# Kernel tuning notes

Measured on AMD Instinct MI355X. Metric: run time of the kernel, lower is better.

The kernel has to match this reference:

```python
import jax, jax.numpy as jnp
import numpy as np
import math

D_INNER = 512
D_STATE = 16
DT_RANK = 32
B_SZ = 2
L_SEQ = 4096


def setup_inputs() -> dict:
    key = jax.random.key(0)
    ks = jax.random.split(key, 6)
    x = jax.random.normal(ks[0], (B_SZ, L_SEQ, D_INNER), dtype=jnp.float32)
    # parameters (match torch init semantics closely enough for a numeric baseline)
    A = jnp.arange(1, D_STATE + 1, dtype=jnp.float32)
    A_log = jnp.broadcast_to(jnp.log(A)[None, :], (D_INNER, D_STATE)).copy()
    D_param = jnp.ones((D_INNER,), dtype=jnp.float32)
    # x_proj: Linear(d_inner -> dt_rank + 2*d_state), no bias
    W_xproj = jax.random.normal(ks[1], (DT_RANK + 2 * D_STATE, D_INNER), dtype=jnp.float32) / np.sqrt(D_INNER)
    # dt_proj: Linear(dt_rank -> d_inner) with special bias init
    W_dt = jax.random.normal(ks[2], (D_INNER, DT_RANK), dtype=jnp.float32) / np.sqrt(DT_RANK)
    dt_init = jnp.exp(jax.random.uniform(ks[3], (D_INNER,)) * (math.log(0.1) - math.log(0.001)) + math.log(0.001))
    b_dt = jnp.log(jnp.exp(dt_init) - 1.0)
    alpha = jnp.asarray(0.6, dtype=jnp.float32)
    beta_logit = jnp.asarray(math.log(0.99 / (1.0 - 0.99 + 1e-08)), dtype=jnp.float32)
    return {"x": x, "A_log": A_log, "D_param": D_param, "W_xproj": W_xproj,
            "W_dt": W_dt, "b_dt": b_dt, "alpha": alpha, "beta_logit": beta_logit}


def _momentum_ssm(x, A_log, D_param, W_xproj, W_dt, b_dt, alpha, beta_logit):
    # x: (B, L, D)
    proj = jnp.einsum('bld,pd->blp', x, W_xproj)            # (B, L, r+2N)
    dt_in = proj[..., :DT_RANK]
    Bp = proj[..., DT_RANK:DT_RANK + D_STATE]                # (B, L, N)
    Cp = proj[..., DT_RANK + D_STATE:]                       # (B, L, N)
    dt = jax.nn.softplus(jnp.einsum('blr,dr->bld', dt_in, W_dt) + b_dt)  # (B, L, D)
    A = -jnp.exp(A_log)                                      # (D, N)
    A_bar = jnp.exp(dt[..., None] * A[None, None])           # (B, L, D, N)
    # fused B_bar * x_t: dt * Bp * x
    inp = dt[..., None] * Bp[:, :, None, :] * x[..., None]   # (B, L, D, N)
    beta = jax.nn.sigmoid(beta_logit)

    # scan over time; carry (h, v): (B, D, N)
    h0 = jnp.zeros((x.shape[0], D_INNER, D_STATE), dtype=x.dtype)
    v0 = jnp.zeros_like(h0)

    def step(carry, ts):
        h, v = carry
        a_t, inp_t, c_t = ts                                 # (B,D,N), (B,D,N), (B,N)
        v = beta * v + alpha * inp_t
        h = a_t * h + v
        y = jnp.einsum('bdn,bn->bd', h, c_t)
        return (h, v), y

    xs = (jnp.moveaxis(A_bar, 1, 0), jnp.moveaxis(inp, 1, 0), jnp.moveaxis(Cp, 1, 0))
    _, ys = jax.lax.scan(step, (h0, v0), xs)                 # ys: (L, B, D)
    y = jnp.moveaxis(ys, 0, 1)                               # (B, L, D)
    return y + D_param * x


def reference(x, A_log, D_param, W_xproj, W_dt, b_dt, alpha, beta_logit):
    return _momentum_ssm(x, A_log, D_param, W_xproj, W_dt, b_dt, alpha, beta_logit)
```

## Files before the change

### kernel.cpp

```cpp
#include <hip/hip_runtime.h>


#define D_IN 512
#define D_ST 16
#define DTR  32
#define BSZ  2
#define LSEQ 4096
#define PDIM 64
#define NCH  256
#define LCH  (LSEQ / NCH)
#define LOG2E 1.44269504f
#define LN2   0.69314718f

typedef __attribute__((ext_vector_type(8))) short short8;
typedef __attribute__((ext_vector_type(4))) float f32x4;
typedef _Float16 f16;
typedef __attribute__((ext_vector_type(8))) _Float16 f16x8;

__device__ inline float fast_exp2(float x) { return __builtin_amdgcn_exp2f(x); }
__device__ inline float fast_log2(float x) { return __builtin_amdgcn_logf(x); }

__device__ inline unsigned short bf16_rne(float f) {
  unsigned b = __float_as_uint(f);
  return (unsigned short)((b + 0x7fffu + ((b >> 16) & 1u)) >> 16);
}

__device__ inline void cvt8(const float4 u, const float4 v, short8& hi, short8& lo) {
  float f[8] = {u.x, u.y, u.z, u.w, v.x, v.y, v.z, v.w};
#pragma unroll
  for (int i = 0; i < 8; ++i) {
    unsigned short h = bf16_rne(f[i]);
    hi[i] = (short)h;
    float r = f[i] - __uint_as_float((unsigned)h << 16);
    lo[i] = (short)bf16_rne(r);
  }
}

__device__ inline void st16h(f16* p, const float* s) {
  f16 t[16];
#pragma unroll
  for (int i = 0; i < 16; ++i) t[i] = (f16)s[i];
  *(f16x8*)p = *(f16x8*)&t[0];
  *(f16x8*)(p + 8) = *(f16x8*)&t[8];
}
__device__ inline void ld16h(const f16* p, float* d) {
  f16x8 a = *(const f16x8*)p;
  f16x8 b = *(const f16x8*)(p + 8);
#pragma unroll
  for (int i = 0; i < 8; ++i) { d[i] = (float)a[i]; d[8 + i] = (float)b[i]; }
}

#define PWCHK(val, n)                                                        \
  pw = pw && (fabsf((val) - (float)((n) + 1) * a0) <=                        \
              2e-5f * fabsf((float)((n) + 1) * a0));

__device__ inline bool detectA2(const float* __restrict__ A_log, int d, float& a0) {
  const float4* ap = (const float4*)(A_log + (size_t)d * D_ST);
  float4 r0 = ap[0], r1 = ap[1], r2 = ap[2], r3 = ap[3];
  float4 e0 = make_float4(-__expf(r0.x) * LOG2E, -__expf(r0.y) * LOG2E,
                          -__expf(r0.z) * LOG2E, -__expf(r0.w) * LOG2E);
  float4 e1 = make_float4(-__expf(r1.x) * LOG2E, -__expf(r1.y) * LOG2E,
                          -__expf(r1.z) * LOG2E, -__expf(r1.w) * LOG2E);
  float4 e2 = make_float4(-__expf(r2.x) * LOG2E, -__expf(r2.y) * LOG2E,
                          -__expf(r2.z) * LOG2E, -__expf(r2.w) * LOG2E);
  float4 e3 = make_float4(-__expf(r3.x) * LOG2E, -__expf(r3.y) * LOG2E,
                          -__expf(r3.z) * LOG2E, -__expf(r3.w) * LOG2E);
  a0 = e0.x;
  bool pw = true;
  PWCHK(e0.y, 1) PWCHK(e0.z, 2) PWCHK(e0.w, 3)
  PWCHK(e1.x, 4) PWCHK(e1.y, 5) PWCHK(e1.z, 6) PWCHK(e1.w, 7)
  PWCHK(e2.x, 8) PWCHK(e2.y, 9) PWCHK(e2.z, 10) PWCHK(e2.w, 11)
  PWCHK(e3.x, 12) PWCHK(e3.y, 13) PWCHK(e3.z, 14) PWCHK(e3.w, 15)
  return pw;
}

__global__ __launch_bounds__(256) void k_wprep(const float* __restrict__ W,
                                               short* __restrict__ Whi,
                                               short* __restrict__ Wlo) {
  const int i = (blockIdx.x * 256 + threadIdx.x) * 4;
  float4 w = *(const float4*)(W + i);
  float f[4] = {w.x, w.y, w.z, w.w};
  unsigned short h[4], lo[4];
#pragma unroll
  for (int j = 0; j < 4; ++j) {
    h[j] = bf16_rne(f[j]);
    float r = f[j] - __uint_as_float((unsigned)h[j] << 16);
    lo[j] = bf16_rne(r);
  }
  *(uint2*)(Whi + i) = make_uint2(h[0] | ((unsigned)h[1] << 16), h[2] | ((unsigned)h[3] << 16));
  *(uint2*)(Wlo + i) = make_uint2(lo[0] | ((unsigned)lo[1] << 16), lo[2] | ((unsigned)lo[3] << 16));
}

#define MM3(ACC, AH, AL, BH, BL)                                        \
  ACC = __builtin_amdgcn_mfma_f32_16x16x32_bf16(AL, BH, ACC, 0, 0, 0);  \
  ACC = __builtin_amdgcn_mfma_f32_16x16x32_bf16(AH, BL, ACC, 0, 0, 0);  \
  ACC = __builtin_amdgcn_mfma_f32_16x16x32_bf16(AH, BH, ACC, 0, 0, 0);

#define LOADB(P, S)                                   \
  {                                                   \
    const int kb = (S) * 32;                          \
    P##h0 = *(const short8*)(bh + kb);                \
    P##h1 = *(const short8*)(bh + 8192 + kb);         \
    P##h2 = *(const short8*)(bh + 16384 + kb);        \
    P##h3 = *(const short8*)(bh + 24576 + kb);        \
    P##l0 = *(const short8*)(bl + kb);                \
    P##l1 = *(const short8*)(bl + 8192 + kb);         \
    P##l2 = *(const short8*)(bl + 16384 + kb);        \
    P##l3 = *(const short8*)(bl + 24576 + kb);        \
  }

#define LOADA(Aa, Ab, S)                              \
  {                                                   \
    const int ka = (S) * 32;                          \
    Aa = *(const float4*)(xr + ka);                   \
    Ab = *(const float4*)(xr + ka + 4);               \
  }

#define COMPSTEP(Aa, Ab, P)                           \
  {                                                   \
    short8 ahi, alo;                                  \
    cvt8(Aa, Ab, ahi, alo);                           \
    MM3(acc0, ahi, alo, P##h0, P##l0);                \
    MM3(acc1, ahi, alo, P##h1, P##l1);                \
    MM3(acc2, ahi, alo, P##h2, P##l2);                \
    MM3(acc3, ahi, alo, P##h3, P##l3);                \
  }

__global__ __launch_bounds__(256) void k_proj(const float* __restrict__ x,
                                              const short* __restrict__ Whi,
                                              const short* __restrict__ Wlo,
                                              float* __restrict__ proj) {
  __shared__ float Pacc[4][16][64];
  const int row0 = blockIdx.x * 16;
  const int l = threadIdx.x & 63;
  const int wq = threadIdx.x >> 6;
  const int m = l & 15;
  const int ko = (l >> 4) * 8 + wq * 128;
  const float* xr = x + (size_t)(row0 + m) * D_IN + ko;
  const short* bh = Whi + (size_t)m * D_IN + ko;
  const short* bl = Wlo + (size_t)m * D_IN + ko;

  f32x4 acc0 = {0.f, 0.f, 0.f, 0.f}, acc1 = acc0, acc2 = acc0, acc3 = acc0;
  float4 A0a, A0b, A1a, A1b, A2a, A2b, A3a, A3b;
  short8 Xh0, Xh1, Xh2, Xh3, Xl0, Xl1, Xl2, Xl3;
  short8 Yh0, Yh1, Yh2, Yh3, Yl0, Yl1, Yl2, Yl3;
  LOADA(A0a, A0b, 0); LOADA(A1a, A1b, 1); LOADA(A2a, A2b, 2); LOADA(A3a, A3b, 3);
  LOADB(X, 0); LOADB(Y, 1);

  COMPSTEP(A0a, A0b, X); LOADB(X, 2);
  COMPSTEP(A1a, A1b, Y); LOADB(Y, 3);
  COMPSTEP(A2a, A2b, X);
  COMPSTEP(A3a, A3b, Y);

  const int r0 = (l >> 4) * 4;
#pragma unroll
  for (int r = 0; r < 4; ++r) {
    Pacc[wq][r0 + r][m] = acc0[r];
    Pacc[wq][r0 + r][16 + m] = acc1[r];
    Pacc[wq][r0 + r][32 + m] = acc2[r];
    Pacc[wq][r0 + r][48 + m] = acc3[r];
  }
  __syncthreads();

  const int orow = threadIdx.x >> 4;
  const int ocol = (threadIdx.x & 15) * 4;
  float4 s0 = *(const float4*)&Pacc[0][orow][ocol];
  float4 s1 = *(const float4*)&Pacc[1][orow][ocol];
  float4 s2 = *(const float4*)&Pacc[2][orow][ocol];
  float4 s3 = *(const float4*)&Pacc[3][orow][ocol];
  float4 o = make_float4((s0.x + s1.x) + (s2.x + s3.x), (s0.y + s1.y) + (s2.y + s3.y),
                         (s0.z + s1.z) + (s2.z + s3.z), (s0.w + s1.w) + (s2.w + s3.w));
  *(float4*)(proj + (size_t)(row0 + orow) * PDIM + ocol) = o;
}

#define S1_LOOP                                                              \
  _Pragma("unroll")                                                          \
  for (int j = 0; j < LCH; ++j) {                                            \
    const float4* pj = (const float4*)(pb + j * PDIM);                       \
    float4 pp[8];                                                            \
    _Pragma("unroll")                                                        \
    for (int k = 0; k < 8; ++k) pp[k] = pj[k];                               \
    float c0 = bb, c1 = 0.f, c2 = 0.f, c3 = 0.f;                             \
    _Pragma("unroll")                                                        \
    for (int k = 0; k < 8; ++k) {                                            \
      c0 = fmaf(pp[k].x, w4[k].x, c0);                                       \
      c1 = fmaf(pp[k].y, w4[k].y, c1);                                       \
      c2 = fmaf(pp[k].z, w4[k].z, c2);                                       \
      c3 = fmaf(pp[k].w, w4[k].w, c3);                                       \
    }                                                                        \
    const float acc = (c0 + c1) + (c2 + c3);                                 \
    const float ee = fast_exp2(acc * LOG2E);                                 \
    const float dtc = (acc > 20.f) ? acc : LN2 * fast_log2(1.f + ee);        \
    dp[(size_t)j * D_IN] = (f16)dtc;                                         \
    sd += dtc;                                                               \
    bpow *= beta;                                                            \
    const float u = alpha * dtc * xs[j];                                     \
    float4 bq[4];                                                            \
    _Pragma("unroll")                                                        \
    for (int k = 0; k < 4; ++k) bq[k] = pj[8 + k];                           \
    const float* Bf = (const float*)bq;                                      \
    AR_INIT;                                                                 \
    _Pragma("unroll")                                                        \
    for (int n = 0; n < 16; ++n) {                                           \
      AR_STEP;                                                               \
      v[n] = fmaf(beta, v[n], u * Bf[n]);                                    \
      h[n] = fmaf(ar, h[n], v[n]);                                           \
      cv[n] = fmaf(ar, cv[n], bpow);                                         \
    }                                                                        \
  }

__global__ __launch_bounds__(256) void k_scan1(const float* __restrict__ x,
                                               const float* __restrict__ proj,
                                               const float* __restrict__ A_log,
                                               const float* __restrict__ W_dt,
                                               const float* __restrict__ b_dt,
                                               const float* __restrict__ alpha_p,
                                               const float* __restrict__ beta_p,
                                               f16* __restrict__ hh,
                                               f16* __restrict__ vh,
                                               f16* __restrict__ cvv,
                                               float* __restrict__ sdt,
                                               f16* __restrict__ dth) {
  const int c = blockIdx.x, b = blockIdx.z;
  const int d = blockIdx.y * 256 + threadIdx.x;
  const int t0 = c * LCH;
  const float* pb = proj + ((size_t)b * LSEQ + t0) * PDIM;

  float xs[LCH];
  {
    const float* xp = x + ((size_t)b * LSEQ + t0) * D_IN + d;
#pragma unroll
    for (int j = 0; j < LCH; ++j) xs[j] = xp[(size_t)j * D_IN];
  }
  float4 w4[8];
  {
    const float4* wp = (const float4*)(W_dt + (size_t)d * DTR);
#pragma unroll
    for (int i = 0; i < 8; ++i) w4[i] = wp[i];
  }
  const float bb = b_dt[d];
  const float alpha = alpha_p[0];
  const float beta = 1.f / (1.f + __expf(-beta_p[0]));
  float a0;
  const bool pw = detectA2(A_log, d, a0);

  f16* dp = dth + ((size_t)b * LSEQ + t0) * D_IN + d;
  float h[16] = {}, v[16] = {}, cv[16] = {};
  float bpow = 1.f, sd = 0.f;

  if (pw) {
#define AR_INIT const float r = fast_exp2(dtc * a0); float ar = 1.f
#define AR_STEP ar *= r
    S1_LOOP
#undef AR_INIT
#undef AR_STEP
  } else {
    volatile const float* av = A_log + (size_t)d * D_ST;
#define AR_INIT float ar
#define AR_STEP ar = fast_exp2(dtc * (-__expf(av[n]) * LOG2E))
    S1_LOOP
#undef AR_INIT
#undef AR_STEP
  }

  const size_t base = ((size_t)(b * NCH + c) * D_IN + d) * D_ST;
  st16h(hh + base, h);
  st16h(vh + base, v);
  st16h(cvv + base, cv);
  sdt[(size_t)(b * NCH + c) * D_IN + d] = sd;
}

__global__ __launch_bounds__(64) void k_fix(f16* __restrict__ hh,
                                            f16* __restrict__ vh,
                                            const f16* __restrict__ cvv,
                                            const float* __restrict__ sdt,
                                            const float* __restrict__ A_log,
                                            const float* __restrict__ beta_p) {
  const int g = blockIdx.x * 64 + threadIdx.x;
  const int b = g >> 13;
  const int dn = g & 8191;
  const float beta = 1.f / (1.f + __expf(-beta_p[0]));
  const float A2 = -__expf(A_log[dn]) * LOG2E;
  float bL = beta;
#pragma unroll
  for (int i = 0; i < 4; ++i) bL *= bL;

  const size_t cs = (size_t)D_IN * D_ST;
  const size_t base = (size_t)b * NCH * cs + dn;
  const size_t sbase = (size_t)b * NCH * D_IN + (dn >> 4);

  float hg[16], vg[16], cg[16], sg[16];
#pragma unroll
  for (int i = 0; i < 16; ++i) {
    hg[i] = (float)hh[base + i * cs];
    vg[i] = (float)vh[base + i * cs];
    cg[i] = (float)cvv[base + i * cs];
    sg[i] = sdt[sbase + i * D_IN];
  }
  float H = 0.f, V = 0.f;
  for (int c0 = 0; c0 < NCH; c0 += 16) {
    const int cp = (c0 + 16) & (NCH - 1);
    float hn[16], vn[16], cn[16], sn[16];
#pragma unroll
    for (int i = 0; i < 16; ++i) {
      hn[i] = (float)hh[base + (size_t)(cp + i) * cs];
      vn[i] = (float)vh[base + (size_t)(cp + i) * cs];
      cn[i] = (float)cvv[base + (size_t)(cp + i) * cs];
      sn[i] = sdt[sbase + (size_t)(cp + i) * D_IN];
    }
#pragma unroll
    for (int i = 0; i < 16; ++i) {
      hh[base + (size_t)(c0 + i) * cs] = (f16)H;
      vh[base + (size_t)(c0 + i) * cs] = (f16)V;
      const float Pa = fast_exp2(sg[i] * A2);
      const float Hn = fmaf(Pa, H, fmaf(cg[i], V, hg[i]));
      V = fmaf(bL, V, vg[i]);
      H = Hn;
    }
#pragma unroll
    for (int i = 0; i < 16; ++i) { hg[i] = hn[i]; vg[i] = vn[i]; cg[i] = cn[i]; sg[i] = sn[i]; }
  }
}

#define S2_LOOP                                                              \
  _Pragma("unroll")                                                          \
  for (int j = 0; j < LCH; ++j) {                                            \
    const float4* pj = (const float4*)(pb + j * PDIM);                       \
    float4 bq[8];                                                            \
    _Pragma("unroll")                                                        \
    for (int k = 0; k < 8; ++k) bq[k] = pj[8 + k];                           \
    const float* Bf = (const float*)bq;                                      \
    const float dtc = dtv[j], xv = xs[j];                                    \
    const float u = alpha * dtc * xv;                                        \
    float y0 = 0.f, y1 = 0.f, y2 = 0.f, y3 = 0.f;                            \
    AR_INIT;                                                                 \
    _Pragma("unroll")                                                        \
    for (int n = 0; n < 16; ++n) {                                           \
      AR_STEP;                                                               \
      v[n] = fmaf(beta, v[n], u * Bf[n]);                                    \
      h[n] = fmaf(ar, h[n], v[n]);                                           \
      float hc = h[n] * Bf[16 + n];                                          \
      if ((n & 3) == 0) y0 += hc;                                            \
      else if ((n & 3) == 1) y1 += hc;                                       \
      else if ((n & 3) == 2) y2 += hc;                                       \
      else y3 += hc;                                                         \
    }                                                                        \
    op[(size_t)j * D_IN] = (y0 + y1) + (y2 + y3) + Dv * xv;                  \
  }

__global__ __launch_bounds__(256) void k_scan2(const float* __restrict__ x,
                                               const f16* __restrict__ dth,
                                               const float* __restrict__ proj,
                                               const float* __restrict__ A_log,
                                               const float* __restrict__ D_param,
                                               const float* __restrict__ alpha_p,
                                               const float* __restrict__ beta_p,
                                               const f16* __restrict__ hh,
                                               const f16* __restrict__ vh,
                                               float* __restrict__ out) {
  const int c = blockIdx.x, b = blockIdx.z;
  const int d = blockIdx.y * 256 + threadIdx.x;
  const int t0 = c * LCH;
  const float* pb = proj + ((size_t)b * LSEQ + t0) * PDIM;

  float xs[LCH], dtv[LCH];
  {
    const float* xp = x + ((size_t)b * LSEQ + t0) * D_IN + d;
    const f16* dp = dth + ((size_t)b * LSEQ + t0) * D_IN + d;
#pragma unroll
    for (int j = 0; j < LCH; ++j) xs[j] = xp[(size_t)j * D_IN];
#pragma unroll
    for (int j = 0; j < LCH; ++j) dtv[j] = (float)dp[(size_t)j * D_IN];
  }
  const float alpha = alpha_p[0];
  const float beta = 1.f / (1.f + __expf(-beta_p[0]));
  const float Dv = D_param[d];
  float a0;
  const bool pw = detectA2(A_log, d, a0);
  const size_t ibase = ((size_t)(b * NCH + c) * D_IN + d) * D_ST;
  float h[16], v[16];
  ld16h(hh + ibase, h);
  ld16h(vh + ibase, v);

  float* op = out + ((size_t)b * LSEQ + t0) * D_IN + d;
  if (pw) {
#define AR_INIT const float r = fast_exp2(dtc * a0); float ar = 1.f
#define AR_STEP ar *= r
    S2_LOOP
#undef AR_INIT
#undef AR_STEP
  } else {
    volatile const float* av = A_log + (size_t)d * D_ST;
#define AR_INIT float ar
#define AR_STEP ar = fast_exp2(dtc * (-__expf(av[n]) * LOG2E))
    S2_LOOP
#undef AR_INIT
#undef AR_STEP
  }
}

extern "C" void kernel_launch(void* const* d_in, const int* in_sizes, int n_in,
                              void* d_out, int out_size, void* d_ws, size_t ws_size,
                              hipStream_t stream) {
  const float* x = (const float*)d_in[0];
  const float* A_log = (const float*)d_in[1];
  const float* D_param = (const float*)d_in[2];
  const float* W_xproj = (const float*)d_in[3];
  const float* W_dt = (const float*)d_in[4];
  const float* b_dt = (const float*)d_in[5];
  const float* alpha = (const float*)d_in[6];
  const float* beta_logit = (const float*)d_in[7];
  float* out = (float*)d_out;

  const size_t NST = (size_t)BSZ * NCH * D_IN * D_ST;
  float* ws = (float*)d_ws;
  float* proj = ws;
  float* sdt = proj + (size_t)BSZ * LSEQ * PDIM;
  f16* hh = (f16*)(sdt + (size_t)BSZ * NCH * D_IN);
  f16* vh = hh + NST;
  f16* cvv = vh + NST;
  f16* dth = cvv + NST;
  short* Whi = (short*)(dth + (size_t)BSZ * LSEQ * D_IN);
  short* Wlo = Whi + (size_t)PDIM * D_IN;

  k_wprep<<<dim3(PDIM * D_IN / 1024), dim3(256), 0, stream>>>(W_xproj, Whi, Wlo);
  k_proj<<<dim3(BSZ * LSEQ / 16), dim3(256), 0, stream>>>(x, Whi, Wlo, proj);
  k_scan1<<<dim3(NCH, D_IN / 256, BSZ), dim3(256), 0, stream>>>(
      x, proj, A_log, W_dt, b_dt, alpha, beta_logit, hh, vh, cvv, sdt, dth);
  k_fix<<<dim3(BSZ * D_IN * D_ST / 64), dim3(64), 0, stream>>>(hh, vh, cvv, sdt, A_log,
                                                               beta_logit);
  k_scan2<<<dim3(NCH, D_IN / 256, BSZ), dim3(256), 0, stream>>>(
      x, dth, proj, A_log, D_param, alpha, beta_logit, hh, vh, out);
}
```

Measured before the change: 167.8 us.

## Fuse x_proj GEMM into both chunked scan kernels via shared memory

Removes the standalone projection kernel and its global proj buffer. Each scan block now handles all 512 channels of one chunk with 512 threads, computes the 16x64 projection tile for its chunk using split-bf16 MFMA into shared memory, then reads B/C/dt_in from LDS. The projection is recomputed in both scan passes, trading extra MFMA work and a block-level sync against one kernel launch and a global round trip. Block count halves while block size doubles, which changes occupancy.

```diff
diff --git a/kernel.cpp b/kernel.cpp
--- a/kernel.cpp
+++ b/kernel.cpp
@@ -96,87 +96,48 @@
   ACC = __builtin_amdgcn_mfma_f32_16x16x32_bf16(AH, BL, ACC, 0, 0, 0);  \
   ACC = __builtin_amdgcn_mfma_f32_16x16x32_bf16(AH, BH, ACC, 0, 0, 0);
 
-#define LOADB(P, S)                                   \
-  {                                                   \
-    const int kb = (S) * 32;                          \
-    P##h0 = *(const short8*)(bh + kb);                \
-    P##h1 = *(const short8*)(bh + 8192 + kb);         \
-    P##h2 = *(const short8*)(bh + 16384 + kb);        \
-    P##h3 = *(const short8*)(bh + 24576 + kb);        \
-    P##l0 = *(const short8*)(bl + kb);                \
-    P##l1 = *(const short8*)(bl + 8192 + kb);         \
-    P##l2 = *(const short8*)(bl + 16384 + kb);        \
-    P##l3 = *(const short8*)(bl + 24576 + kb);        \
-  }
-
-#define LOADA(Aa, Ab, S)                              \
-  {                                                   \
-    const int ka = (S) * 32;                          \
-    Aa = *(const float4*)(xr + ka);                   \
-    Ab = *(const float4*)(xr + ka + 4);               \
-  }
-
-#define COMPSTEP(Aa, Ab, P)                           \
-  {                                                   \
-    short8 ahi, alo;                                  \
-    cvt8(Aa, Ab, ahi, alo);                           \
-    MM3(acc0, ahi, alo, P##h0, P##l0);                \
-    MM3(acc1, ahi, alo, P##h1, P##l1);                \
-    MM3(acc2, ahi, alo, P##h2, P##l2);                \
-    MM3(acc3, ahi, alo, P##h3, P##l3);                \
-  }
-
-__global__ __launch_bounds__(256) void k_proj(const float* __restrict__ x,
-                                              const short* __restrict__ Whi,
-                                              const short* __restrict__ Wlo,
-                                              float* __restrict__ proj) {
-  __shared__ float Pacc[4][16][64];
-  const int row0 = blockIdx.x * 16;
+__device__ inline void stage_proj(const float* __restrict__ x,
+                                  const short* __restrict__ Whi,
+                                  const short* __restrict__ Wlo,
+                                  int b, int t0,
+                                  float (*Pacc)[16][64], float (*Ps)[64]) {
   const int l = threadIdx.x & 63;
-  const int wq = threadIdx.x >> 6;
+  const int w = threadIdx.x >> 6;
+  const int q = w & 3, kh = w >> 2;
   const int m = l & 15;
-  const int ko = (l >> 4) * 8 + wq * 128;
-  const float* xr = x + (size_t)(row0 + m) * D_IN + ko;
-  const short* bh = Whi + (size_t)m * D_IN + ko;
-  const short* bl = Wlo + (size_t)m * D_IN + ko;
-
-  f32x4 acc0 = {0.f, 0.f, 0.f, 0.f}, acc1 = acc0, acc2 = acc0, acc3 = acc0;
-  float4 A0a, A0b, A1a, A1b, A2a, A2b, A3a, A3b;
-  short8 Xh0, Xh1, Xh2, Xh3, Xl0, Xl1, Xl2, Xl3;
-  short8 Yh0, Yh1, Yh2, Yh3, Yl0, Yl1, Yl2, Yl3;
-  LOADA(A0a, A0b, 0); LOADA(A1a, A1b, 1); LOADA(A2a, A2b, 2); LOADA(A3a, A3b, 3);
-  LOADB(X, 0); LOADB(Y, 1);
-
-  COMPSTEP(A0a, A0b, X); LOADB(X, 2);
-  COMPSTEP(A1a, A1b, Y); LOADB(Y, 3);
-  COMPSTEP(A2a, A2b, X);
-  COMPSTEP(A3a, A3b, Y);
-
+  const int ko = (l >> 4) * 8 + kh * 256;
+  const float* xr = x + ((size_t)b * LSEQ + t0 + m) * D_IN + ko;
+  const short* bh = Whi + (size_t)(q * 16 + m) * D_IN + ko;
+  const short* bl = Wlo + (size_t)(q * 16 + m) * D_IN + ko;
+
+  f32x4 acc = {0.f, 0.f, 0.f, 0.f};
+#pragma unroll
+  for (int s = 0; s < 8; ++s) {
+    float4 Aa = *(const float4*)(xr + s * 32);
+    float4 Ab = *(const float4*)(xr + s * 32 + 4);
+    short8 ahi, alo;
+    cvt8(Aa, Ab, ahi, alo);
+    short8 Bh = *(const short8*)(bh + s * 32);
+    short8 Bl = *(const short8*)(bl + s * 32);
+    MM3(acc, ahi, alo, Bh, Bl);
+  }
   const int r0 = (l >> 4) * 4;
 #pragma unroll
-  for (int r = 0; r < 4; ++r) {
-    Pacc[wq][r0 + r][m] = acc0[r];
-    Pacc[wq][r0 + r][16 + m] = acc1[r];
-    Pacc[wq][r0 + r][32 + m] = acc2[r];
-    Pacc[wq][r0 + r][48 + m] = acc3[r];
-  }
+  for (int r = 0; r < 4; ++r) Pacc[kh][r0 + r][q * 16 + m] = acc[r];
   __syncthreads();
-
-  const int orow = threadIdx.x >> 4;
-  const int ocol = (threadIdx.x & 15) * 4;
-  float4 s0 = *(const float4*)&Pacc[0][orow][ocol];
-  float4 s1 = *(const float4*)&Pacc[1][orow][ocol];
-  float4 s2 = *(const float4*)&Pacc[2][orow][ocol];
-  float4 s3 = *(const float4*)&Pacc[3][orow][ocol];
-  float4 o = make_float4((s0.x + s1.x) + (s2.x + s3.x), (s0.y + s1.y) + (s2.y + s3.y),
-                         (s0.z + s1.z) + (s2.z + s3.z), (s0.w + s1.w) + (s2.w + s3.w));
-  *(float4*)(proj + (size_t)(row0 + orow) * PDIM + ocol) = o;
+  {
+    const int o = threadIdx.x * 2;
+    const int row = o >> 6, col = o & 63;
+    Ps[row][col] = Pacc[0][row][col] + Pacc[1][row][col];
+    Ps[row][col + 1] = Pacc[0][row][col + 1] + Pacc[1][row][col + 1];
+  }
+  __syncthreads();
 }
 
 #define S1_LOOP                                                              \
   _Pragma("unroll")                                                          \
   for (int j = 0; j < LCH; ++j) {                                            \
-    const float4* pj = (const float4*)(pb + j * PDIM);                       \
+    const float4* pj = (const float4*)&Ps[j][0];                             \
     float4 pp[8];                                                            \
     _Pragma("unroll")                                                        \
     for (int k = 0; k < 8; ++k) pp[k] = pj[k];                               \
@@ -209,22 +170,26 @@
     }                                                                        \
   }
 
-__global__ __launch_bounds__(256) void k_scan1(const float* __restrict__ x,
-                                               const float* __restrict__ proj,
-                                               const float* __restrict__ A_log,
-                                               const float* __restrict__ W_dt,
-                                               const float* __restrict__ b_dt,
-                                               const float* __restrict__ alpha_p,
-                                               const float* __restrict__ beta_p,
-                                               f16* __restrict__ hh,
-                                               f16* __restrict__ vh,
-                                               f16* __restrict__ cvv,
-                                               float* __restrict__ sdt,
-                                               f16* __restrict__ dth) {
+__global__ __launch_bounds__(512) void k_scan1f(const float* __restrict__ x,
+                                                const short* __restrict__ Whi,
+                                                const short* __restrict__ Wlo,
+                                                const float* __restrict__ A_log,
+                                                const float* __restrict__ W_dt,
+                                                const float* __restrict__ b_dt,
+                                                const float* __restrict__ alpha_p,
+                                                const float* __restrict__ beta_p,
+                                                f16* __restrict__ hh,
+                                                f16* __restrict__ vh,
+                                                f16* __restrict__ cvv,
+                                                float* __restrict__ sdt,
+                                                f16* __restrict__ dth) {
+  __shared__ float Pacc[2][16][64];
+  __shared__ float Ps[16][64];
   const int c = blockIdx.x, b = blockIdx.z;
-  const int d = blockIdx.y * 256 + threadIdx.x;
+  const int d = threadIdx.x;
   const int t0 = c * LCH;
-  const float* pb = proj + ((size_t)b * LSEQ + t0) * PDIM;
+
+  stage_proj(x, Whi, Wlo, b, t0, Pacc, Ps);
 
   float xs[LCH];
   {
@@ -325,7 +290,7 @@
 #define S2_LOOP                                                              \
   _Pragma("unroll")                                                          \
   for (int j = 0; j < LCH; ++j) {                                            \
-    const float4* pj = (const float4*)(pb + j * PDIM);                       \
+    const float4* pj = (const float4*)&Ps[j][0];                             \
     float4 bq[8];                                                            \
     _Pragma("unroll")                                                        \
     for (int k = 0; k < 8; ++k) bq[k] = pj[8 + k];                           \
@@ -348,20 +313,24 @@
     op[(size_t)j * D_IN] = (y0 + y1) + (y2 + y3) + Dv * xv;                  \
   }
 
-__global__ __launch_bounds__(256) void k_scan2(const float* __restrict__ x,
-                                               const f16* __restrict__ dth,
-                                               const float* __restrict__ proj,
-                                               const float* __restrict__ A_log,
-                                               const float* __restrict__ D_param,
-                                               const float* __restrict__ alpha_p,
-                                               const float* __restrict__ beta_p,
-                                               const f16* __restrict__ hh,
-                                               const f16* __restrict__ vh,
-                                               float* __restrict__ out) {
+__global__ __launch_bounds__(512) void k_scan2f(const float* __restrict__ x,
+                                                const short* __restrict__ Whi,
+                                                const short* __restrict__ Wlo,
+                                                const f16* __restrict__ dth,
+                                                const float* __restrict__ A_log,
+                                                const float* __restrict__ D_param,
+                                                const float* __restrict__ alpha_p,
+                                                const float* __restrict__ beta_p,
+                                                const f16* __restrict__ hh,
+                                                const f16* __restrict__ vh,
+                                                float* __restrict__ out) {
+  __shared__ float Pacc[2][16][64];
+  __shared__ float Ps[16][64];
   const int c = blockIdx.x, b = blockIdx.z;
-  const int d = blockIdx.y * 256 + threadIdx.x;
+  const int d = threadIdx.x;
   const int t0 = c * LCH;
-  const float* pb = proj + ((size_t)b * LSEQ + t0) * PDIM;
+
+  stage_proj(x, Whi, Wlo, b, t0, Pacc, Ps);
 
   float xs[LCH], dtv[LCH];
   {
@@ -414,8 +383,7 @@
 
   const size_t NST = (size_t)BSZ * NCH * D_IN * D_ST;
   float* ws = (float*)d_ws;
-  float* proj = ws;
-  float* sdt = proj + (size_t)BSZ * LSEQ * PDIM;
+  float* sdt = ws;
   f16* hh = (f16*)(sdt + (size_t)BSZ * NCH * D_IN);
   f16* vh = hh + NST;
   f16* cvv = vh + NST;
@@ -424,11 +392,10 @@
   short* Wlo = Whi + (size_t)PDIM * D_IN;
 
   k_wprep<<<dim3(PDIM * D_IN / 1024), dim3(256), 0, stream>>>(W_xproj, Whi, Wlo);
-  k_proj<<<dim3(BSZ * LSEQ / 16), dim3(256), 0, stream>>>(x, Whi, Wlo, proj);
-  k_scan1<<<dim3(NCH, D_IN / 256, BSZ), dim3(256), 0, stream>>>(
-      x, proj, A_log, W_dt, b_dt, alpha, beta_logit, hh, vh, cvv, sdt, dth);
+  k_scan1f<<<dim3(NCH, 1, BSZ), dim3(512), 0, stream>>>(
+      x, Whi, Wlo, A_log, W_dt, b_dt, alpha, beta_logit, hh, vh, cvv, sdt, dth);
   k_fix<<<dim3(BSZ * D_IN * D_ST / 64), dim3(64), 0, stream>>>(hh, vh, cvv, sdt, A_log,
                                                                beta_logit);
-  k_scan2<<<dim3(NCH, D_IN / 256, BSZ), dim3(256), 0, stream>>>(
-      x, dth, proj, A_log, D_param, alpha, beta_logit, hh, vh, out);
-}
+  k_scan2f<<<dim3(NCH, 1, BSZ), dim3(512), 0, stream>>>(
+      x, Whi, Wlo, dth, A_log, D_param, alpha, beta_logit, hh, vh, out);
+}
```

Result: slower. 181.6 us (+8.2%).
